# Kernel tuning notes

Hardware: AMD Instinct MI355X
Metric: run time of the kernel (lower is better)

The kernel has to match this reference:

```python
import jax, jax.numpy as jnp
import numpy as np

L = 4          # dilation_depth
HID = 32       # hidden_channels
F_IN = 16
F_OUT = 16
K = 2          # conv kernel size


def setup_inputs() -> dict:
    key = jax.random.key(0)
    ks = jax.random.split(key, 20)
    B, T, N, F = 8, 512, 128, F_IN
    s = 0.1
    inp = {
        "X": jax.random.normal(ks[0], (B, T, N, F), jnp.float32),
        "A": jax.random.normal(ks[1], (N, N), jnp.float32) / jnp.sqrt(N).astype(jnp.float32),
        "in_w": jax.random.normal(ks[2], (F, 3 * HID), jnp.float32) * s,
        "in_b": jnp.zeros((3 * HID,), jnp.float32),
        "ct_w": jax.random.normal(ks[3], (L, K, HID, HID), jnp.float32) * s,
        "ct_b": jnp.zeros((L, HID), jnp.float32),
        "cs_w": jax.random.normal(ks[4], (L, K, HID, HID), jnp.float32) * s,
        "cs_b": jnp.zeros((L, HID), jnp.float32),
        "gcn_w": jax.random.normal(ks[5], (L, HID, HID), jnp.float32) * s,
        "gcn_b": jnp.zeros((L, HID), jnp.float32),
        "res_w": jax.random.normal(ks[6], (L, HID, HID), jnp.float32) * s,
        "res_b": jnp.zeros((L, HID), jnp.float32),
        "skip_w": jax.random.normal(ks[7], (L, HID, HID), jnp.float32) * s,
        "skip_b": jnp.zeros((L, HID), jnp.float32),
        "out1_w": jax.random.normal(ks[8], (HID, HID), jnp.float32) * s,
        "out1_b": jnp.zeros((HID,), jnp.float32),
        "out2_w": jax.random.normal(ks[9], (HID, F_OUT), jnp.float32) * s,
        "out2_b": jnp.zeros((F_OUT,), jnp.float32),
    }
    return inp


def _causal_conv(x, w, b, dilation):
    # x: [BN, T, C]; w: [K, C_in, C_out] (WIO); causal pad left by dilation*(K-1)
    pad = dilation * (w.shape[0] - 1)
    y = jax.lax.conv_general_dilated(
        x, w, window_strides=(1,), padding=[(pad, 0)],
        rhs_dilation=(dilation,), dimension_numbers=("NWC", "WIO", "NWC"))
    return y + b


def reference(X, A, in_w, in_b, ct_w, ct_b, cs_w, cs_b, gcn_w, gcn_b,
              res_w, res_b, skip_w, skip_b, out1_w, out1_b, out2_w, out2_b):
    B, T, N, F = X.shape
    Xp = X @ in_w + in_b                      # [B,T,N,3H]
    x_a, x_b, x_res = jnp.split(Xp, 3, axis=-1)
    H = x_a.shape[-1]
    # Faithful to source: raw reshape [B,T,N,H] -> [B*N,T,H] (no transpose), as in the original code.
    x_a_r = x_a.reshape(B * N, T, H)
    x_b_r = x_b.reshape(B * N, T, H)
    skip = jnp.zeros_like(x_res)
    for i in range(L):
        d = 2 ** i
        tcn = (jnp.tanh(_causal_conv(x_a_r, ct_w[i], ct_b[i], d))
               * jax.nn.sigmoid(_causal_conv(x_b_r, cs_w[i], cs_b[i], d)))
        tcn = tcn.reshape(B, N, T, H).transpose(0, 2, 1, 3)   # [B,T,N,H]
        gcn = jnp.einsum('ij,btjf->btif', A, x_res) @ gcn_w[i] + gcn_b[i]
        h = tcn + gcn
        x_res = (h @ res_w[i] + res_b[i]) + x_res
        skip = skip + (h @ skip_w[i] + skip_b[i])
    h = jax.nn.relu(skip)
    h = jax.nn.relu(h @ out1_w + out1_b)
    return h @ out2_w + out2_b
```

## Files before the change

kernel.cpp:

```cpp
#include <hip/hip_runtime.h>
#include <math.h>

#define T_ 512

typedef _Float16 half8 __attribute__((ext_vector_type(8)));
typedef float f32x4 __attribute__((ext_vector_type(4)));

__device__ __forceinline__ float sigm(float x)  { return 1.0f / (1.0f + __expf(-x)); }
__device__ __forceinline__ float tanhf_(float x){ return 1.0f - 2.0f / (1.0f + __expf(2.0f * x)); }

__global__ __launch_bounds__(256) void k_prep(
    const float* __restrict__ A,     const float* __restrict__ in_w,
    const float* __restrict__ in_b,
    const float* __restrict__ ct_w,  const float* __restrict__ ct_b,
    const float* __restrict__ cs_w,  const float* __restrict__ cs_b,
    const float* __restrict__ gcn_w, const float* __restrict__ res_w,
    const float* __restrict__ skip_w,
    const float* __restrict__ out1_w,const float* __restrict__ out2_w,
    _Float16* __restrict__ AF, _Float16* __restrict__ WF, float* __restrict__ BIAS)
{
    int idx = blockIdx.x * 256 + threadIdx.x;
    if (idx < 16384) {
        int j = idx & 7, L = (idx >> 3) & 63, tile = idx >> 9;
        int mt = tile >> 2, kt = tile & 3;
        int m = mt * 16 + (L & 15), k = kt * 32 + (L >> 4) * 8 + j;
        AF[idx] = (_Float16)A[m * 128 + k];
    } else if (idx < 39936) {
        int e = idx - 16384;
        int j = e & 7, L = (e >> 3) & 63, nt = (e >> 9) & 1, mat = e >> 10;
        int k = (L >> 4) * 8 + j, n = nt * 16 + (L & 15);
        float v = 0.f;
        if (mat < 20) {
            int l = mat / 5, r = mat - l * 5;
            if (r <= 1) {
                const float* tw = (r == 0 ? ct_w : cs_w) + l * 2048;
                int bro = r * 32;
                if (k < 16) {
                    for (int c = 0; c < 32; ++c) v += in_w[k*96 + bro + c] * tw[c*32 + n];
                } else {
                    for (int c = 0; c < 32; ++c) v += in_w[(k-16)*96 + bro + c] * tw[1024 + c*32 + n];
                }
            } else if (r == 2) v = gcn_w [l*1024 + k*32 + n];
            else if   (r == 3) v = res_w [l*1024 + k*32 + n];
            else               v = skip_w[l*1024 + k*32 + n];
        } else if (mat == 20) v = out1_w[k*32 + n];
        else if   (mat == 21) v = (n < 16) ? out2_w[k*16 + n] : 0.f;
        else                  v = (k >= 16) ? in_w[(k-16)*96 + 64 + n] : 0.f;
        WF[e] = (_Float16)v;
    } else if (idx < 40448) {
        int e = idx - 39936;
        int n = e & 31, q = (e >> 5) & 3, l = e >> 7;
        float v = 0.f;
        if (q == 0) { v = ct_b[l*32+n]; for (int c = 0; c < 32; ++c) v += in_b[c]      * ct_w[l*2048 + 1024 + c*32 + n]; }
        else if (q == 1) {              for (int c = 0; c < 32; ++c) v += in_b[c]      * ct_w[l*2048 +        c*32 + n]; }
        else if (q == 2) { v = cs_b[l*32+n]; for (int c = 0; c < 32; ++c) v += in_b[32+c] * cs_w[l*2048 + 1024 + c*32 + n]; }
        else {                          for (int c = 0; c < 32; ++c) v += in_b[32+c]   * cs_w[l*2048 +        c*32 + n]; }
        BIAS[l*128 + q*32 + n] = v;
    }
}

__global__ __launch_bounds__(256, 3) void k_fused(
    const float* __restrict__ X,
    const _Float16* __restrict__ AF,
    const _Float16* __restrict__ WF,
    const float* __restrict__ BIAS,
    const float* __restrict__ in_b,
    const float* __restrict__ gcn_b,
    const float* __restrict__ res_b,
    const float* __restrict__ skip_b,
    const float* __restrict__ b1,
    const float* __restrict__ b2,
    float* __restrict__ out)
{
    __shared__ _Float16 Pld [128 * 40];
    __shared__ _Float16 hsld[128 * 40];
    __shared__ _Float16 xsT [2][32 * 136];

    const int btid = blockIdx.x;
    const int b = btid >> 9, t = btid & (T_ - 1);
    const int tid = threadIdx.x, lane = tid & 63, w = tid >> 6;
    const int lm = lane & 15, kb = lane >> 4;
    const int R = w * 32;

    const half8* AFv = (const half8*)AF;
    const half8* WFv = (const half8*)WF;
    const f32x4 zero4 = {0.f, 0.f, 0.f, 0.f};

    half8 Af[2][4];
#pragma unroll
    for (int mt = 0; mt < 2; ++mt)
#pragma unroll
        for (int kt = 0; kt < 4; ++kt)
            Af[mt][kt] = AFv[((w * 2 + mt) * 4 + kt) * 64 + lane];

    float xm[2][2][4];
    float sk[2][2][4];
#pragma unroll
    for (int mt = 0; mt < 2; ++mt)
#pragma unroll
        for (int nt = 0; nt < 2; ++nt)
#pragma unroll
            for (int r = 0; r < 4; ++r) sk[mt][nt][r] = 0.f;

    {
        int row = R + (lane >> 1);
        int cur = lane & 1;
        half8 h0 = {0,0,0,0,0,0,0,0}, h1 = {0,0,0,0,0,0,0,0};
        if (cur) {
            const float4* s4 = (const float4*)(X + ((size_t)btid * 128 + row) * 16);
            float v[16];
#pragma unroll
            for (int k = 0; k < 4; ++k) {
                float4 u = s4[k];
                v[4*k+0] = u.x; v[4*k+1] = u.y; v[4*k+2] = u.z; v[4*k+3] = u.w;
            }
#pragma unroll
            for (int k = 0; k < 8; ++k) { h0[k] = (_Float16)v[k]; h1[k] = (_Float16)v[8 + k]; }
        }
        *(half8*)&hsld[row * 40 + cur * 16]     = h0;
        *(half8*)&hsld[row * 40 + cur * 16 + 8] = h1;
    }
    __syncthreads();
    {
        half8 pt[2];
#pragma unroll
        for (int mt = 0; mt < 2; ++mt)
            pt[mt] = *(const half8*)&hsld[(R + mt * 16 + lm) * 40 + kb * 8];
#pragma unroll
        for (int nt = 0; nt < 2; ++nt) {
            half8 wi = WFv[(22 * 2 + nt) * 64 + lane];
            float bi = in_b[64 + nt * 16 + lm];
#pragma unroll
            for (int mt = 0; mt < 2; ++mt) {
                f32x4 di = __builtin_amdgcn_mfma_f32_16x16x32_f16(pt[mt], wi, zero4, 0, 0, 0);
#pragma unroll
                for (int r = 0; r < 4; ++r) xm[mt][nt][r] = di[r] + bi;
            }
        }
    }
    __syncthreads();

#pragma unroll 1
    for (int l = 0; l < 4; ++l) {
        const int d = 1 << l;
        const bool pv = (t >= d);

        {
            int row = R + (lane >> 1);
            int cur = lane & 1;
            size_t q = (size_t)(b * 128 + row) * T_ + t - (cur ? 0 : d);
            float v[16];
            if (cur || pv) {
                const float4* s4 = (const float4*)(X + q * 16);
#pragma unroll
                for (int k = 0; k < 4; ++k) {
                    float4 u = s4[k];
                    v[4*k+0] = u.x; v[4*k+1] = u.y; v[4*k+2] = u.z; v[4*k+3] = u.w;
                }
            } else {
#pragma unroll
                for (int k = 0; k < 16; ++k) v[k] = 0.f;
            }
            half8 h0, h1;
#pragma unroll
            for (int k = 0; k < 8; ++k) { h0[k] = (_Float16)v[k]; h1[k] = (_Float16)v[8 + k]; }
            *(half8*)&Pld[row * 40 + cur * 16]     = h0;
            *(half8*)&Pld[row * 40 + cur * 16 + 8] = h1;
        }
        __syncthreads();

        half8 pf[2];
#pragma unroll
        for (int mt = 0; mt < 2; ++mt)
            pf[mt] = *(const half8*)&Pld[(R + mt * 16 + lm) * 40 + kb * 8];

        f32x4 Dt[2][2], Ds[2][2];
#pragma unroll
        for (int nt = 0; nt < 2; ++nt) {
            half8 wt = WFv[((l * 5 + 0) * 2 + nt) * 64 + lane];
            half8 ws = WFv[((l * 5 + 1) * 2 + nt) * 64 + lane];
#pragma unroll
            for (int mt = 0; mt < 2; ++mt) {
                Dt[mt][nt] = __builtin_amdgcn_mfma_f32_16x16x32_f16(pf[mt], wt, zero4, 0, 0, 0);
                Ds[mt][nt] = __builtin_amdgcn_mfma_f32_16x16x32_f16(pf[mt], ws, zero4, 0, 0, 0);
            }
        }
        float tc[2][2][4];
#pragma unroll
        for (int nt = 0; nt < 2; ++nt) {
            int n = nt * 16 + lm;
            float bt = BIAS[l*128 +      n] + (pv ? BIAS[l*128 + 32 + n] : 0.f);
            float bs = BIAS[l*128 + 64 + n] + (pv ? BIAS[l*128 + 96 + n] : 0.f);
#pragma unroll
            for (int mt = 0; mt < 2; ++mt)
#pragma unroll
                for (int r = 0; r < 4; ++r)
                    tc[mt][nt][r] = tanhf_(Dt[mt][nt][r] + bt) * sigm(Ds[mt][nt][r] + bs);
        }

        {
            _Float16* xp = xsT[l & 1];
#pragma unroll
            for (int mt = 0; mt < 2; ++mt)
#pragma unroll
                for (int nt = 0; nt < 2; ++nt)
#pragma unroll
                    for (int r = 0; r < 4; ++r)
                        xp[(nt * 16 + lm) * 136 + R + mt * 16 + kb * 4 + r] =
                            (_Float16)xm[mt][nt][r];
        }
        __syncthreads();

        f32x4 AxD[2][2];
#pragma unroll
        for (int nt = 0; nt < 2; ++nt) {
            half8 Bx[4];
#pragma unroll
            for (int kt = 0; kt < 4; ++kt)
                Bx[kt] = *(const half8*)&xsT[l & 1][(nt * 16 + lm) * 136 + kt * 32 + kb * 8];
#pragma unroll
            for (int mt = 0; mt < 2; ++mt) {
                f32x4 acc = zero4;
#pragma unroll
                for (int kt = 0; kt < 4; ++kt)
                    acc = __builtin_amdgcn_mfma_f32_16x16x32_f16(Af[mt][kt], Bx[kt], acc, 0, 0, 0);
                AxD[mt][nt] = acc;
            }
        }
#pragma unroll
        for (int mt = 0; mt < 2; ++mt)
#pragma unroll
            for (int nt = 0; nt < 2; ++nt)
#pragma unroll
                for (int r = 0; r < 4; ++r)
                    hsld[(R + mt * 16 + kb * 4 + r) * 40 + nt * 16 + lm] =
                        (_Float16)AxD[mt][nt][r];
        __syncthreads();

        half8 ha[2];
#pragma unroll
        for (int mt = 0; mt < 2; ++mt)
            ha[mt] = *(const half8*)&hsld[(R + mt * 16 + lm) * 40 + kb * 8];
        f32x4 hD[2][2];
#pragma unroll
        for (int nt = 0; nt < 2; ++nt) {
            half8 wg = WFv[((l * 5 + 2) * 2 + nt) * 64 + lane];
            float gb = gcn_b[l * 32 + nt * 16 + lm];
#pragma unroll
            for (int mt = 0; mt < 2; ++mt) {
                f32x4 acc = __builtin_amdgcn_mfma_f32_16x16x32_f16(ha[mt], wg, zero4, 0, 0, 0);
#pragma unroll
                for (int r = 0; r < 4; ++r) hD[mt][nt][r] = acc[r] + gb + tc[mt][nt][r];
            }
        }
        __syncthreads();
#pragma unroll
        for (int mt = 0; mt < 2; ++mt)
#pragma unroll
            for (int nt = 0; nt < 2; ++nt)
#pragma unroll
                for (int r = 0; r < 4; ++r)
                    hsld[(R + mt * 16 + kb * 4 + r) * 40 + nt * 16 + lm] =
                        (_Float16)hD[mt][nt][r];
        __syncthreads();

        half8 hh[2];
#pragma unroll
        for (int mt = 0; mt < 2; ++mt)
            hh[mt] = *(const half8*)&hsld[(R + mt * 16 + lm) * 40 + kb * 8];
#pragma unroll
        for (int nt = 0; nt < 2; ++nt) {
            half8 wr = WFv[((l * 5 + 3) * 2 + nt) * 64 + lane];
            half8 wsk= WFv[((l * 5 + 4) * 2 + nt) * 64 + lane];
            float rb = res_b [l * 32 + nt * 16 + lm];
            float sb = skip_b[l * 32 + nt * 16 + lm];
#pragma unroll
            for (int mt = 0; mt < 2; ++mt) {
                f32x4 rD = __builtin_amdgcn_mfma_f32_16x16x32_f16(hh[mt], wr,  zero4, 0, 0, 0);
                f32x4 sD = __builtin_amdgcn_mfma_f32_16x16x32_f16(hh[mt], wsk, zero4, 0, 0, 0);
#pragma unroll
                for (int r = 0; r < 4; ++r) {
                    xm[mt][nt][r] += rD[r] + rb;
                    sk[mt][nt][r] += sD[r] + sb;
                }
            }
        }
    }

    __syncthreads();
#pragma unroll
    for (int mt = 0; mt < 2; ++mt)
#pragma unroll
        for (int nt = 0; nt < 2; ++nt)
#pragma unroll
            for (int r = 0; r < 4; ++r)
                hsld[(R + mt * 16 + kb * 4 + r) * 40 + nt * 16 + lm] =
                    (_Float16)fmaxf(sk[mt][nt][r], 0.f);
    __syncthreads();

    half8 sf[2];
#pragma unroll
    for (int mt = 0; mt < 2; ++mt)
        sf[mt] = *(const half8*)&hsld[(R + mt * 16 + lm) * 40 + kb * 8];
    f32x4 h1D[2][2];
#pragma unroll
    for (int nt = 0; nt < 2; ++nt) {
        half8 w1f = WFv[(20 * 2 + nt) * 64 + lane];
        float bb = b1[nt * 16 + lm];
#pragma unroll
        for (int mt = 0; mt < 2; ++mt) {
            f32x4 acc = __builtin_amdgcn_mfma_f32_16x16x32_f16(sf[mt], w1f, zero4, 0, 0, 0);
#pragma unroll
            for (int r = 0; r < 4; ++r) h1D[mt][nt][r] = fmaxf(acc[r] + bb, 0.f);
        }
    }
    __syncthreads();
#pragma unroll
    for (int mt = 0; mt < 2; ++mt)
#pragma unroll
        for (int nt = 0; nt < 2; ++nt)
#pragma unroll
            for (int r = 0; r < 4; ++r)
                hsld[(R + mt * 16 + kb * 4 + r) * 40 + nt * 16 + lm] =
                    (_Float16)h1D[mt][nt][r];
    __syncthreads();

    half8 hf[2];
#pragma unroll
    for (int mt = 0; mt < 2; ++mt)
        hf[mt] = *(const half8*)&hsld[(R + mt * 16 + lm) * 40 + kb * 8];
    {
        half8 w2f = WFv[(21 * 2 + 0) * 64 + lane];
        float bb = b2[lm];
#pragma unroll
        for (int mt = 0; mt < 2; ++mt) {
            f32x4 o = __builtin_amdgcn_mfma_f32_16x16x32_f16(hf[mt], w2f, zero4, 0, 0, 0);
#pragma unroll
            for (int r = 0; r < 4; ++r)
                out[((size_t)btid * 128 + R + mt * 16 + kb * 4 + r) * 16 + lm] = o[r] + bb;
        }
    }
}

extern "C" void kernel_launch(void* const* d_in, const int* in_sizes, int n_in,
                              void* d_out, int out_size, void* d_ws, size_t ws_size,
                              hipStream_t stream)
{
    const float* X      = (const float*)d_in[0];
    const float* A      = (const float*)d_in[1];
    const float* in_w   = (const float*)d_in[2];
    const float* in_b   = (const float*)d_in[3];
    const float* ct_w   = (const float*)d_in[4];
    const float* ct_b   = (const float*)d_in[5];
    const float* cs_w   = (const float*)d_in[6];
    const float* cs_b   = (const float*)d_in[7];
    const float* gcn_w  = (const float*)d_in[8];
    const float* gcn_b  = (const float*)d_in[9];
    const float* res_w  = (const float*)d_in[10];
    const float* res_b  = (const float*)d_in[11];
    const float* skip_w = (const float*)d_in[12];
    const float* skip_b = (const float*)d_in[13];
    const float* out1_w = (const float*)d_in[14];
    const float* out1_b = (const float*)d_in[15];
    const float* out2_w = (const float*)d_in[16];
    const float* out2_b = (const float*)d_in[17];

    char* ws = (char*)d_ws;
    _Float16* AF   = (_Float16*)ws;
    _Float16* WF   = (_Float16*)(ws + 32768);
    float*    BIAS = (float*)   (ws + 32768 + 47104);

    k_prep<<<158, 256, 0, stream>>>(A, in_w, in_b, ct_w, ct_b, cs_w, cs_b,
                                    gcn_w, res_w, skip_w, out1_w, out2_w,
                                    AF, WF, BIAS);

    k_fused<<<8 * T_, 256, 0, stream>>>(X, AF, WF, BIAS, in_b,
                                        gcn_b, res_b, skip_b,
                                        out1_b, out2_b, (float*)d_out);
}
```

Baseline: 241.4 us.

## Keep activations in MFMA registers using transposed 16x16x16 chaining, drop LDS round trips

Rewrites the per-layer dataflow so MFMA accumulator outputs feed the next matmul directly as 16x16x16 fragments. It alternates between normal and transposed products, which removes the hsld shared buffer and most __syncthreads between the GCN, residual and skip stages. The weight prep kernel emits a new fragment layout with half4 K-split tiles for the 32x32 weights. The A fragments are now reloaded inside each layer, and output stores become float4 writes. This cuts LDS traffic and barriers per layer, at the cost of more register pressure and repeated global/L2 loads of the A fragments.

```diff
diff --git a/kernel.cpp b/kernel.cpp
--- a/kernel.cpp
+++ b/kernel.cpp
@@ -4,10 +4,18 @@
 #define T_ 512
 
 typedef _Float16 half8 __attribute__((ext_vector_type(8)));
+typedef _Float16 half4 __attribute__((ext_vector_type(4)));
 typedef float f32x4 __attribute__((ext_vector_type(4)));
 
 __device__ __forceinline__ float sigm(float x)  { return 1.0f / (1.0f + __expf(-x)); }
 __device__ __forceinline__ float tanhf_(float x){ return 1.0f - 2.0f / (1.0f + __expf(2.0f * x)); }
+
+__device__ __forceinline__ half4 pack4(f32x4 v) {
+    half4 h;
+    h[0] = (_Float16)v[0]; h[1] = (_Float16)v[1];
+    h[2] = (_Float16)v[2]; h[3] = (_Float16)v[3];
+    return h;
+}
 
 __global__ __launch_bounds__(256) void k_prep(
     const float* __restrict__ A,     const float* __restrict__ in_w,
@@ -17,52 +25,55 @@
     const float* __restrict__ gcn_w, const float* __restrict__ res_w,
     const float* __restrict__ skip_w,
     const float* __restrict__ out1_w,const float* __restrict__ out2_w,
-    _Float16* __restrict__ AF, _Float16* __restrict__ WF, float* __restrict__ BIAS)
+    _Float16* __restrict__ FR, float* __restrict__ BIAS)
 {
     int idx = blockIdx.x * 256 + threadIdx.x;
     if (idx < 16384) {
         int j = idx & 7, L = (idx >> 3) & 63, tile = idx >> 9;
-        int mt = tile >> 2, kt = tile & 3;
-        int m = mt * 16 + (L & 15), k = kt * 32 + (L >> 4) * 8 + j;
-        AF[idx] = (_Float16)A[m * 128 + k];
+        int it = tile >> 2, kt = tile & 3;
+        FR[idx] = (_Float16)A[(it * 16 + (L & 15)) * 128 + kt * 32 + (L >> 4) * 8 + j];
+    } else if (idx < 25600) {
+        int e = idx - 16384;
+        int j = e & 7, L = (e >> 3) & 63, ct = (e >> 9) & 1, mat = e >> 10;
+        int k = (L >> 4) * 8 + j, col = ct * 16 + (L & 15);
+        float v = 0.f;
+        if (mat < 8) {
+            int l = mat >> 1, br = mat & 1;
+            const float* tw = (br ? cs_w : ct_w) + l * 2048;
+            int bro = br * 32;
+            if (k < 16) { for (int c = 0; c < 32; ++c) v += in_w[k*96 + bro + c] * tw[c*32 + col]; }
+            else        { for (int c = 0; c < 32; ++c) v += in_w[(k-16)*96 + bro + c] * tw[1024 + c*32 + col]; }
+        } else {
+            v = (k >= 16) ? in_w[(k - 16) * 96 + 64 + col] : 0.f;
+        }
+        FR[idx] = (_Float16)v;
     } else if (idx < 39936) {
-        int e = idx - 16384;
-        int j = e & 7, L = (e >> 3) & 63, nt = (e >> 9) & 1, mat = e >> 10;
-        int k = (L >> 4) * 8 + j, n = nt * 16 + (L & 15);
-        float v = 0.f;
-        if (mat < 20) {
-            int l = mat / 5, r = mat - l * 5;
-            if (r <= 1) {
-                const float* tw = (r == 0 ? ct_w : cs_w) + l * 2048;
-                int bro = r * 32;
-                if (k < 16) {
-                    for (int c = 0; c < 32; ++c) v += in_w[k*96 + bro + c] * tw[c*32 + n];
-                } else {
-                    for (int c = 0; c < 32; ++c) v += in_w[(k-16)*96 + bro + c] * tw[1024 + c*32 + n];
-                }
-            } else if (r == 2) v = gcn_w [l*1024 + k*32 + n];
-            else if   (r == 3) v = res_w [l*1024 + k*32 + n];
-            else               v = skip_w[l*1024 + k*32 + n];
-        } else if (mat == 20) v = out1_w[k*32 + n];
-        else if   (mat == 21) v = (n < 16) ? out2_w[k*16 + n] : 0.f;
-        else                  v = (k >= 16) ? in_w[(k-16)*96 + 64 + n] : 0.f;
-        WF[e] = (_Float16)v;
+        int e = idx - 25600;
+        int i = e & 3, L = (e >> 2) & 63, ct = (e >> 8) & 1, ks = (e >> 9) & 1, mat = e >> 10;
+        int k = ks * 16 + (L >> 4) * 4 + i, col = ct * 16 + (L & 15);
+        float v;
+        if (mat < 12) {
+            int l = mat / 3, r = mat - l * 3;
+            const float* W = (r == 0) ? gcn_w : (r == 1) ? res_w : skip_w;
+            v = W[l * 1024 + k * 32 + col];
+        } else if (mat == 12) v = out1_w[k * 32 + col];
+        else                  v = (ct == 0) ? out2_w[k * 16 + (L & 15)] : 0.f;
+        FR[idx] = (_Float16)v;
     } else if (idx < 40448) {
         int e = idx - 39936;
         int n = e & 31, q = (e >> 5) & 3, l = e >> 7;
         float v = 0.f;
-        if (q == 0) { v = ct_b[l*32+n]; for (int c = 0; c < 32; ++c) v += in_b[c]      * ct_w[l*2048 + 1024 + c*32 + n]; }
-        else if (q == 1) {              for (int c = 0; c < 32; ++c) v += in_b[c]      * ct_w[l*2048 +        c*32 + n]; }
+        if (q == 0) { v = ct_b[l*32+n]; for (int c = 0; c < 32; ++c) v += in_b[c]    * ct_w[l*2048 + 1024 + c*32 + n]; }
+        else if (q == 1) {              for (int c = 0; c < 32; ++c) v += in_b[c]    * ct_w[l*2048 +        c*32 + n]; }
         else if (q == 2) { v = cs_b[l*32+n]; for (int c = 0; c < 32; ++c) v += in_b[32+c] * cs_w[l*2048 + 1024 + c*32 + n]; }
-        else {                          for (int c = 0; c < 32; ++c) v += in_b[32+c]   * cs_w[l*2048 +        c*32 + n]; }
+        else {                          for (int c = 0; c < 32; ++c) v += in_b[32+c] * cs_w[l*2048 +        c*32 + n]; }
         BIAS[l*128 + q*32 + n] = v;
     }
 }
 
 __global__ __launch_bounds__(256, 3) void k_fused(
     const float* __restrict__ X,
-    const _Float16* __restrict__ AF,
-    const _Float16* __restrict__ WF,
+    const _Float16* __restrict__ FR,
     const float* __restrict__ BIAS,
     const float* __restrict__ in_b,
     const float* __restrict__ gcn_b,
@@ -72,9 +83,8 @@
     const float* __restrict__ b2,
     float* __restrict__ out)
 {
-    __shared__ _Float16 Pld [128 * 40];
-    __shared__ _Float16 hsld[128 * 40];
-    __shared__ _Float16 xsT [2][32 * 136];
+    __shared__ _Float16 Pld[128 * 40];
+    __shared__ _Float16 xsT[2][32 * 136];
 
     const int btid = blockIdx.x;
     const int b = btid >> 9, t = btid & (T_ - 1);
@@ -82,63 +92,51 @@
     const int lm = lane & 15, kb = lane >> 4;
     const int R = w * 32;
 
-    const half8* AFv = (const half8*)AF;
-    const half8* WFv = (const half8*)WF;
+    const half8* AFv  = (const half8*)FR;
+    const half8* W32v = (const half8*)(FR + 16384);
+    const half4* W16v = (const half4*)(FR + 25600);
     const f32x4 zero4 = {0.f, 0.f, 0.f, 0.f};
 
-    half8 Af[2][4];
-#pragma unroll
-    for (int mt = 0; mt < 2; ++mt)
-#pragma unroll
-        for (int kt = 0; kt < 4; ++kt)
-            Af[mt][kt] = AFv[((w * 2 + mt) * 4 + kt) * 64 + lane];
-
-    float xm[2][2][4];
-    float sk[2][2][4];
-#pragma unroll
-    for (int mt = 0; mt < 2; ++mt)
-#pragma unroll
-        for (int nt = 0; nt < 2; ++nt)
-#pragma unroll
-            for (int r = 0; r < 4; ++r) sk[mt][nt][r] = 0.f;
+    const int row = lane >> 1, ch = lane & 1;
 
     {
-        int row = R + (lane >> 1);
-        int cur = lane & 1;
-        half8 h0 = {0,0,0,0,0,0,0,0}, h1 = {0,0,0,0,0,0,0,0};
-        if (cur) {
-            const float4* s4 = (const float4*)(X + ((size_t)btid * 128 + row) * 16);
-            float v[16];
-#pragma unroll
-            for (int k = 0; k < 4; ++k) {
-                float4 u = s4[k];
-                v[4*k+0] = u.x; v[4*k+1] = u.y; v[4*k+2] = u.z; v[4*k+3] = u.w;
-            }
-#pragma unroll
-            for (int k = 0; k < 8; ++k) { h0[k] = (_Float16)v[k]; h1[k] = (_Float16)v[8 + k]; }
-        }
-        *(half8*)&hsld[row * 40 + cur * 16]     = h0;
-        *(half8*)&hsld[row * 40 + cur * 16 + 8] = h1;
-    }
-    __syncthreads();
+        const float4* s4 = (const float4*)(X + ((size_t)btid * 128 + R + row) * 16 + ch * 8);
+        float4 u0 = s4[0], u1 = s4[1];
+        half8 hv;
+        hv[0]=(_Float16)u0.x; hv[1]=(_Float16)u0.y; hv[2]=(_Float16)u0.z; hv[3]=(_Float16)u0.w;
+        hv[4]=(_Float16)u1.x; hv[5]=(_Float16)u1.y; hv[6]=(_Float16)u1.z; hv[7]=(_Float16)u1.w;
+        half8 z8 = {0,0,0,0,0,0,0,0};
+        *(half8*)&Pld[(R + row) * 40 + ch * 8]      = z8;
+        *(half8*)&Pld[(R + row) * 40 + 16 + ch * 8] = hv;
+    }
+
+    f32x4 xm[2][2], skT[2][2];
     {
-        half8 pt[2];
-#pragma unroll
-        for (int mt = 0; mt < 2; ++mt)
-            pt[mt] = *(const half8*)&hsld[(R + mt * 16 + lm) * 40 + kb * 8];
-#pragma unroll
-        for (int nt = 0; nt < 2; ++nt) {
-            half8 wi = WFv[(22 * 2 + nt) * 64 + lane];
-            float bi = in_b[64 + nt * 16 + lm];
-#pragma unroll
-            for (int mt = 0; mt < 2; ++mt) {
-                f32x4 di = __builtin_amdgcn_mfma_f32_16x16x32_f16(pt[mt], wi, zero4, 0, 0, 0);
-#pragma unroll
-                for (int r = 0; r < 4; ++r) xm[mt][nt][r] = di[r] + bi;
-            }
-        }
-    }
-    __syncthreads();
+        half8 pt0 = *(const half8*)&Pld[(R + lm) * 40 + kb * 8];
+        half8 pt1 = *(const half8*)&Pld[(R + 16 + lm) * 40 + kb * 8];
+#pragma unroll
+        for (int f = 0; f < 2; ++f) {
+            half8 wi = W32v[(8 * 2 + f) * 64 + lane];
+            float bi = in_b[64 + f * 16 + lm];
+            f32x4 d0 = __builtin_amdgcn_mfma_f32_16x16x32_f16(pt0, wi, zero4, 0, 0, 0);
+            f32x4 d1 = __builtin_amdgcn_mfma_f32_16x16x32_f16(pt1, wi, zero4, 0, 0, 0);
+#pragma unroll
+            for (int r = 0; r < 4; ++r) { xm[0][f][r] = d0[r] + bi; xm[1][f][r] = d1[r] + bi; }
+        }
+#pragma unroll
+        for (int a = 0; a < 2; ++a)
+#pragma unroll
+            for (int c = 0; c < 2; ++c) skT[a][c] = zero4;
+    }
+
+    {
+        const float4* s4 = (const float4*)(X + ((size_t)(b * 128 + R + row) * T_ + t) * 16 + ch * 8);
+        float4 u0 = s4[0], u1 = s4[1];
+        half8 hv;
+        hv[0]=(_Float16)u0.x; hv[1]=(_Float16)u0.y; hv[2]=(_Float16)u0.z; hv[3]=(_Float16)u0.w;
+        hv[4]=(_Float16)u1.x; hv[5]=(_Float16)u1.y; hv[6]=(_Float16)u1.z; hv[7]=(_Float16)u1.w;
+        *(half8*)&Pld[(R + row) * 40 + 16 + ch * 8] = hv;
+    }
 
 #pragma unroll 1
     for (int l = 0; l < 4; ++l) {
@@ -146,198 +144,154 @@
         const bool pv = (t >= d);
 
         {
-            int row = R + (lane >> 1);
-            int cur = lane & 1;
-            size_t q = (size_t)(b * 128 + row) * T_ + t - (cur ? 0 : d);
-            float v[16];
-            if (cur || pv) {
-                const float4* s4 = (const float4*)(X + q * 16);
-#pragma unroll
-                for (int k = 0; k < 4; ++k) {
-                    float4 u = s4[k];
-                    v[4*k+0] = u.x; v[4*k+1] = u.y; v[4*k+2] = u.z; v[4*k+3] = u.w;
-                }
-            } else {
-#pragma unroll
-                for (int k = 0; k < 16; ++k) v[k] = 0.f;
-            }
-            half8 h0, h1;
-#pragma unroll
-            for (int k = 0; k < 8; ++k) { h0[k] = (_Float16)v[k]; h1[k] = (_Float16)v[8 + k]; }
-            *(half8*)&Pld[row * 40 + cur * 16]     = h0;
-            *(half8*)&Pld[row * 40 + cur * 16 + 8] = h1;
-        }
+            half8 hv = {0,0,0,0,0,0,0,0};
+            if (pv) {
+                const float4* s4 = (const float4*)(X + ((size_t)(b * 128 + R + row) * T_ + (t - d)) * 16 + ch * 8);
+                float4 u0 = s4[0], u1 = s4[1];
+                hv[0]=(_Float16)u0.x; hv[1]=(_Float16)u0.y; hv[2]=(_Float16)u0.z; hv[3]=(_Float16)u0.w;
+                hv[4]=(_Float16)u1.x; hv[5]=(_Float16)u1.y; hv[6]=(_Float16)u1.z; hv[7]=(_Float16)u1.w;
+            }
+            *(half8*)&Pld[(R + row) * 40 + ch * 8] = hv;
+        }
+
+        half8 pf0 = *(const half8*)&Pld[(R + lm) * 40 + kb * 8];
+        half8 pf1 = *(const half8*)&Pld[(R + 16 + lm) * 40 + kb * 8];
+        f32x4 tcv[2][2];
+#pragma unroll
+        for (int ct = 0; ct < 2; ++ct) {
+            half8 wt = W32v[((l * 2 + 0) * 2 + ct) * 64 + lane];
+            half8 ws = W32v[((l * 2 + 1) * 2 + ct) * 64 + lane];
+            f32x4 dt0 = __builtin_amdgcn_mfma_f32_16x16x32_f16(wt, pf0, zero4, 0, 0, 0);
+            f32x4 dt1 = __builtin_amdgcn_mfma_f32_16x16x32_f16(wt, pf1, zero4, 0, 0, 0);
+            f32x4 ds0 = __builtin_amdgcn_mfma_f32_16x16x32_f16(ws, pf0, zero4, 0, 0, 0);
+            f32x4 ds1 = __builtin_amdgcn_mfma_f32_16x16x32_f16(ws, pf1, zero4, 0, 0, 0);
+            const float4 bt0 = *(const float4*)&BIAS[l*128 +       ct*16 + kb*4];
+            const float4 bt1 = *(const float4*)&BIAS[l*128 + 32 +  ct*16 + kb*4];
+            const float4 bs0 = *(const float4*)&BIAS[l*128 + 64 +  ct*16 + kb*4];
+            const float4 bs1 = *(const float4*)&BIAS[l*128 + 96 +  ct*16 + kb*4];
+            float btq[4] = { bt0.x + (pv ? bt1.x : 0.f), bt0.y + (pv ? bt1.y : 0.f),
+                             bt0.z + (pv ? bt1.z : 0.f), bt0.w + (pv ? bt1.w : 0.f) };
+            float bsq[4] = { bs0.x + (pv ? bs1.x : 0.f), bs0.y + (pv ? bs1.y : 0.f),
+                             bs0.z + (pv ? bs1.z : 0.f), bs0.w + (pv ? bs1.w : 0.f) };
+#pragma unroll
+            for (int r = 0; r < 4; ++r) {
+                tcv[ct][0][r] = tanhf_(dt0[r] + btq[r]) * sigm(ds0[r] + bsq[r]);
+                tcv[ct][1][r] = tanhf_(dt1[r] + btq[r]) * sigm(ds1[r] + bsq[r]);
+            }
+        }
+
+        const int buf = l & 1;
+#pragma unroll
+        for (int mt = 0; mt < 2; ++mt)
+#pragma unroll
+            for (int f = 0; f < 2; ++f)
+                *(half4*)&xsT[buf][(f * 16 + lm) * 136 + R + mt * 16 + kb * 4] = pack4(xm[mt][f]);
         __syncthreads();
 
-        half8 pf[2];
+        f32x4 AxT[2][2];
+        half8 Afr[2][4];
 #pragma unroll
         for (int mt = 0; mt < 2; ++mt)
-            pf[mt] = *(const half8*)&Pld[(R + mt * 16 + lm) * 40 + kb * 8];
-
-        f32x4 Dt[2][2], Ds[2][2];
-#pragma unroll
-        for (int nt = 0; nt < 2; ++nt) {
-            half8 wt = WFv[((l * 5 + 0) * 2 + nt) * 64 + lane];
-            half8 ws = WFv[((l * 5 + 1) * 2 + nt) * 64 + lane];
-#pragma unroll
-            for (int mt = 0; mt < 2; ++mt) {
-                Dt[mt][nt] = __builtin_amdgcn_mfma_f32_16x16x32_f16(pf[mt], wt, zero4, 0, 0, 0);
-                Ds[mt][nt] = __builtin_amdgcn_mfma_f32_16x16x32_f16(pf[mt], ws, zero4, 0, 0, 0);
-            }
-        }
-        float tc[2][2][4];
-#pragma unroll
-        for (int nt = 0; nt < 2; ++nt) {
-            int n = nt * 16 + lm;
-            float bt = BIAS[l*128 +      n] + (pv ? BIAS[l*128 + 32 + n] : 0.f);
-            float bs = BIAS[l*128 + 64 + n] + (pv ? BIAS[l*128 + 96 + n] : 0.f);
-#pragma unroll
-            for (int mt = 0; mt < 2; ++mt)
-#pragma unroll
-                for (int r = 0; r < 4; ++r)
-                    tc[mt][nt][r] = tanhf_(Dt[mt][nt][r] + bt) * sigm(Ds[mt][nt][r] + bs);
-        }
-
-        {
-            _Float16* xp = xsT[l & 1];
-#pragma unroll
-            for (int mt = 0; mt < 2; ++mt)
-#pragma unroll
-                for (int nt = 0; nt < 2; ++nt)
-#pragma unroll
-                    for (int r = 0; r < 4; ++r)
-                        xp[(nt * 16 + lm) * 136 + R + mt * 16 + kb * 4 + r] =
-                            (_Float16)xm[mt][nt][r];
-        }
-        __syncthreads();
-
-        f32x4 AxD[2][2];
-#pragma unroll
-        for (int nt = 0; nt < 2; ++nt) {
-            half8 Bx[4];
 #pragma unroll
             for (int kt = 0; kt < 4; ++kt)
-                Bx[kt] = *(const half8*)&xsT[l & 1][(nt * 16 + lm) * 136 + kt * 32 + kb * 8];
+                Afr[mt][kt] = AFv[((w * 2 + mt) * 4 + kt) * 64 + lane];
+#pragma unroll
+        for (int f = 0; f < 2; ++f) {
+            half8 xa[4];
+#pragma unroll
+            for (int kt = 0; kt < 4; ++kt)
+                xa[kt] = *(const half8*)&xsT[buf][(f * 16 + lm) * 136 + kt * 32 + kb * 8];
 #pragma unroll
             for (int mt = 0; mt < 2; ++mt) {
                 f32x4 acc = zero4;
 #pragma unroll
                 for (int kt = 0; kt < 4; ++kt)
-                    acc = __builtin_amdgcn_mfma_f32_16x16x32_f16(Af[mt][kt], Bx[kt], acc, 0, 0, 0);
-                AxD[mt][nt] = acc;
-            }
-        }
+                    acc = __builtin_amdgcn_mfma_f32_16x16x32_f16(xa[kt], Afr[mt][kt], acc, 0, 0, 0);
+                AxT[f][mt] = acc;
+            }
+        }
+
+        half4 axh[2][2];
+#pragma unroll
+        for (int f = 0; f < 2; ++f)
+#pragma unroll
+            for (int mt = 0; mt < 2; ++mt) axh[f][mt] = pack4(AxT[f][mt]);
+        half4 hh[2][2];
+#pragma unroll
+        for (int g = 0; g < 2; ++g) {
+            half4 gw0 = W16v[((l * 3 + 0) * 4 + 0 * 2 + g) * 64 + lane];
+            half4 gw1 = W16v[((l * 3 + 0) * 4 + 1 * 2 + g) * 64 + lane];
+            const float4 gb = *(const float4*)&gcn_b[l * 32 + g * 16 + kb * 4];
+            float gbq[4] = { gb.x, gb.y, gb.z, gb.w };
+#pragma unroll
+            for (int mt = 0; mt < 2; ++mt) {
+                f32x4 acc = __builtin_amdgcn_mfma_f32_16x16x16f16(gw0, axh[0][mt], zero4, 0, 0, 0);
+                acc = __builtin_amdgcn_mfma_f32_16x16x16f16(gw1, axh[1][mt], acc, 0, 0, 0);
+#pragma unroll
+                for (int r = 0; r < 4; ++r) acc[r] += gbq[r] + tcv[g][mt][r];
+                hh[g][mt] = pack4(acc);
+            }
+        }
+
 #pragma unroll
         for (int mt = 0; mt < 2; ++mt)
 #pragma unroll
-            for (int nt = 0; nt < 2; ++nt)
-#pragma unroll
-                for (int r = 0; r < 4; ++r)
-                    hsld[(R + mt * 16 + kb * 4 + r) * 40 + nt * 16 + lm] =
-                        (_Float16)AxD[mt][nt][r];
-        __syncthreads();
-
-        half8 ha[2];
-#pragma unroll
-        for (int mt = 0; mt < 2; ++mt)
-            ha[mt] = *(const half8*)&hsld[(R + mt * 16 + lm) * 40 + kb * 8];
-        f32x4 hD[2][2];
-#pragma unroll
-        for (int nt = 0; nt < 2; ++nt) {
-            half8 wg = WFv[((l * 5 + 2) * 2 + nt) * 64 + lane];
-            float gb = gcn_b[l * 32 + nt * 16 + lm];
-#pragma unroll
-            for (int mt = 0; mt < 2; ++mt) {
-                f32x4 acc = __builtin_amdgcn_mfma_f32_16x16x32_f16(ha[mt], wg, zero4, 0, 0, 0);
-#pragma unroll
-                for (int r = 0; r < 4; ++r) hD[mt][nt][r] = acc[r] + gb + tc[mt][nt][r];
-            }
-        }
-        __syncthreads();
-#pragma unroll
-        for (int mt = 0; mt < 2; ++mt)
-#pragma unroll
-            for (int nt = 0; nt < 2; ++nt)
-#pragma unroll
-                for (int r = 0; r < 4; ++r)
-                    hsld[(R + mt * 16 + kb * 4 + r) * 40 + nt * 16 + lm] =
-                        (_Float16)hD[mt][nt][r];
-        __syncthreads();
-
-        half8 hh[2];
-#pragma unroll
-        for (int mt = 0; mt < 2; ++mt)
-            hh[mt] = *(const half8*)&hsld[(R + mt * 16 + lm) * 40 + kb * 8];
-#pragma unroll
-        for (int nt = 0; nt < 2; ++nt) {
-            half8 wr = WFv[((l * 5 + 3) * 2 + nt) * 64 + lane];
-            half8 wsk= WFv[((l * 5 + 4) * 2 + nt) * 64 + lane];
-            float rb = res_b [l * 32 + nt * 16 + lm];
-            float sb = skip_b[l * 32 + nt * 16 + lm];
-#pragma unroll
-            for (int mt = 0; mt < 2; ++mt) {
-                f32x4 rD = __builtin_amdgcn_mfma_f32_16x16x32_f16(hh[mt], wr,  zero4, 0, 0, 0);
-                f32x4 sD = __builtin_amdgcn_mfma_f32_16x16x32_f16(hh[mt], wsk, zero4, 0, 0, 0);
-#pragma unroll
-                for (int r = 0; r < 4; ++r) {
-                    xm[mt][nt][r] += rD[r] + rb;
-                    sk[mt][nt][r] += sD[r] + sb;
-                }
-            }
-        }
-    }
-
-    __syncthreads();
-#pragma unroll
-    for (int mt = 0; mt < 2; ++mt)
-#pragma unroll
-        for (int nt = 0; nt < 2; ++nt)
-#pragma unroll
-            for (int r = 0; r < 4; ++r)
-                hsld[(R + mt * 16 + kb * 4 + r) * 40 + nt * 16 + lm] =
-                    (_Float16)fmaxf(sk[mt][nt][r], 0.f);
-    __syncthreads();
-
-    half8 sf[2];
-#pragma unroll
-    for (int mt = 0; mt < 2; ++mt)
-        sf[mt] = *(const half8*)&hsld[(R + mt * 16 + lm) * 40 + kb * 8];
-    f32x4 h1D[2][2];
-#pragma unroll
-    for (int nt = 0; nt < 2; ++nt) {
-        half8 w1f = WFv[(20 * 2 + nt) * 64 + lane];
-        float bb = b1[nt * 16 + lm];
+            for (int f3 = 0; f3 < 2; ++f3) {
+                half4 rw0 = W16v[((l * 3 + 1) * 4 + 0 * 2 + f3) * 64 + lane];
+                half4 rw1 = W16v[((l * 3 + 1) * 4 + 1 * 2 + f3) * 64 + lane];
+                f32x4 acc = __builtin_amdgcn_mfma_f32_16x16x16f16(hh[0][mt], rw0, xm[mt][f3], 0, 0, 0);
+                xm[mt][f3] = __builtin_amdgcn_mfma_f32_16x16x16f16(hh[1][mt], rw1, acc, 0, 0, 0);
+                float rb = res_b[l * 32 + f3 * 16 + lm];
+#pragma unroll
+                for (int r = 0; r < 4; ++r) xm[mt][f3][r] += rb;
+
+                half4 sw0 = W16v[((l * 3 + 2) * 4 + 0 * 2 + f3) * 64 + lane];
+                half4 sw1 = W16v[((l * 3 + 2) * 4 + 1 * 2 + f3) * 64 + lane];
+                f32x4 acs = __builtin_amdgcn_mfma_f32_16x16x16f16(sw0, hh[0][mt], skT[f3][mt], 0, 0, 0);
+                skT[f3][mt] = __builtin_amdgcn_mfma_f32_16x16x16f16(sw1, hh[1][mt], acs, 0, 0, 0);
+                const float4 sb = *(const float4*)&skip_b[l * 32 + f3 * 16 + kb * 4];
+                skT[f3][mt][0] += sb.x; skT[f3][mt][1] += sb.y;
+                skT[f3][mt][2] += sb.z; skT[f3][mt][3] += sb.w;
+            }
+    }
+
+    half4 rs[2][2];
+#pragma unroll
+    for (int g = 0; g < 2; ++g)
 #pragma unroll
         for (int mt = 0; mt < 2; ++mt) {
-            f32x4 acc = __builtin_amdgcn_mfma_f32_16x16x32_f16(sf[mt], w1f, zero4, 0, 0, 0);
-#pragma unroll
-            for (int r = 0; r < 4; ++r) h1D[mt][nt][r] = fmaxf(acc[r] + bb, 0.f);
-        }
-    }
-    __syncthreads();
-#pragma unroll
-    for (int mt = 0; mt < 2; ++mt)
-#pragma unroll
-        for (int nt = 0; nt < 2; ++nt)
-#pragma unroll
-            for (int r = 0; r < 4; ++r)
-                hsld[(R + mt * 16 + kb * 4 + r) * 40 + nt * 16 + lm] =
-                    (_Float16)h1D[mt][nt][r];
-    __syncthreads();
-
-    half8 hf[2];
-#pragma unroll
-    for (int mt = 0; mt < 2; ++mt)
-        hf[mt] = *(const half8*)&hsld[(R + mt * 16 + lm) * 40 + kb * 8];
+            f32x4 v;
+#pragma unroll
+            for (int r = 0; r < 4; ++r) v[r] = fmaxf(skT[g][mt][r], 0.f);
+            rs[g][mt] = pack4(v);
+        }
+    half4 h1h[2][2];
+#pragma unroll
+    for (int g4 = 0; g4 < 2; ++g4) {
+        half4 w10 = W16v[(12 * 4 + 0 * 2 + g4) * 64 + lane];
+        half4 w11 = W16v[(12 * 4 + 1 * 2 + g4) * 64 + lane];
+        const float4 bb = *(const float4*)&b1[g4 * 16 + kb * 4];
+        float bbq[4] = { bb.x, bb.y, bb.z, bb.w };
+#pragma unroll
+        for (int mt = 0; mt < 2; ++mt) {
+            f32x4 acc = __builtin_amdgcn_mfma_f32_16x16x16f16(w10, rs[0][mt], zero4, 0, 0, 0);
+            acc = __builtin_amdgcn_mfma_f32_16x16x16f16(w11, rs[1][mt], acc, 0, 0, 0);
+            f32x4 v;
+#pragma unroll
+            for (int r = 0; r < 4; ++r) v[r] = fmaxf(acc[r] + bbq[r], 0.f);
+            h1h[g4][mt] = pack4(v);
+        }
+    }
     {
-        half8 w2f = WFv[(21 * 2 + 0) * 64 + lane];
-        float bb = b2[lm];
+        half4 w20 = W16v[(13 * 4 + 0 * 2 + 0) * 64 + lane];
+        half4 w21 = W16v[(13 * 4 + 1 * 2 + 0) * 64 + lane];
+        const float4 bb = *(const float4*)&b2[kb * 4];
 #pragma unroll
         for (int mt = 0; mt < 2; ++mt) {
-            f32x4 o = __builtin_amdgcn_mfma_f32_16x16x32_f16(hf[mt], w2f, zero4, 0, 0, 0);
-#pragma unroll
-            for (int r = 0; r < 4; ++r)
-                out[((size_t)btid * 128 + R + mt * 16 + kb * 4 + r) * 16 + lm] = o[r] + bb;
+            f32x4 acc = __builtin_amdgcn_mfma_f32_16x16x16f16(w20, h1h[0][mt], zero4, 0, 0, 0);
+            acc = __builtin_amdgcn_mfma_f32_16x16x16f16(w21, h1h[1][mt], acc, 0, 0, 0);
+            float4 o = make_float4(acc[0] + bb.x, acc[1] + bb.y, acc[2] + bb.z, acc[3] + bb.w);
+            *(float4*)&out[((size_t)btid * 128 + R + mt * 16 + lm) * 16 + kb * 4] = o;
         }
     }
 }
@@ -365,16 +319,14 @@
     const float* out2_w = (const float*)d_in[16];
     const float* out2_b = (const float*)d_in[17];
 
-    char* ws = (char*)d_ws;
-    _Float16* AF   = (_Float16*)ws;
-    _Float16* WF   = (_Float16*)(ws + 32768);
-    float*    BIAS = (float*)   (ws + 32768 + 47104);
+    _Float16* FR   = (_Float16*)d_ws;
+    float*    BIAS = (float*)((char*)d_ws + 79872);
 
     k_prep<<<158, 256, 0, stream>>>(A, in_w, in_b, ct_w, ct_b, cs_w, cs_b,
                                     gcn_w, res_w, skip_w, out1_w, out2_w,
-                                    AF, WF, BIAS);
-
-    k_fused<<<8 * T_, 256, 0, stream>>>(X, AF, WF, BIAS, in_b,
+                                    FR, BIAS);
+
+    k_fused<<<8 * T_, 256, 0, stream>>>(X, FR, BIAS, in_b,
                                         gcn_b, res_b, skip_b,
                                         out1_b, out2_b, (float*)d_out);
 }
```

Measured after the change: 237.2 us. About the same (-1.7%).
